# Kernel tuning notes

Hardware: AMD Instinct MI355X
Metric: run time of the kernel (lower is better)

## Reference

```python
import jax, jax.numpy as jnp
import numpy as np

B, T, D = 32, 2048, 128


def setup_inputs() -> dict:
    key = jax.random.key(0)
    k1, k2, k3 = jax.random.split(key, 3)
    values = jax.random.normal(k1, (B, T, D), dtype=jnp.float32)
    # monotonically increasing per-feature timestamps (irregular sampling)
    times = jnp.cumsum(jax.random.uniform(k2, (B, T, D), dtype=jnp.float32), axis=1)
    mask = jax.random.randint(k3, (B, T, D), 0, 2) > 0  # True = observed
    return {"values": values, "times": times, "mask": mask}


def _fill(x, t, mask):
    """Parallel forward fill (LOCF) and backward fill (NOCB) of x and t.

    Replaces the serial Keras RNN scan with cummax/cummin over observation
    indices followed by a gather. Matches ForwardCell semantics:
      forward : x init 0, t init times[:, 0, :]
      backward: x init 0, t init max(times, axis=1)
    """
    Tn = x.shape[1]
    ar = jnp.broadcast_to(jnp.arange(Tn, dtype=jnp.int32)[None, :, None], x.shape)
    # ---- forward fill ----
    fidx = jax.lax.cummax(jnp.where(mask, ar, -1), axis=1)  # last observed idx
    fvalid = fidx >= 0
    fi = jnp.clip(fidx, 0, Tn - 1)
    x_last = jnp.where(fvalid, jnp.take_along_axis(x, fi, axis=1), 0.0)
    t_last = jnp.where(fvalid, jnp.take_along_axis(t, fi, axis=1), t[:, :1, :])
    # ---- backward fill ----
    bidx = jax.lax.cummin(jnp.where(mask, ar, Tn), axis=1, reverse=True)  # next observed idx
    bvalid = bidx < Tn
    bi = jnp.clip(bidx, 0, Tn - 1)
    x_next = jnp.where(bvalid, jnp.take_along_axis(x, bi, axis=1), 0.0)
    t_next = jnp.where(bvalid, jnp.take_along_axis(t, bi, axis=1),
                       jnp.max(t, axis=1, keepdims=True))
    return x_last, t_last, x_next, t_next


def reference(values, times, mask):
    x_last, t_last, x_next, t_next = _fill(values, times, mask)
    denom = t_next - t_last
    num = x_last * (t_next - times) + x_next * (times - t_last)
    safe = denom != 0.0
    x_itp = num / jnp.where(safe, denom, 1.0)
    x_itp = jnp.where(safe & jnp.isfinite(x_itp), x_itp, 0.0)  # nan/inf -> 0
    return jnp.where(mask, values, x_itp)
```

## Files before the change

kernel.cpp:

```cpp
#include <hip/hip_runtime.h>
#include <math.h>

constexpr int B   = 32;
constexpr int T   = 2048;
constexpr int D   = 128;
constexpr int C   = 8;
constexpr int NCH = T / C;
constexpr int DG  = D / 4;

__global__ __launch_bounds__(256)
void linterp_kernel(const float* __restrict__ values,
                    const float* __restrict__ times,
                    const int*   __restrict__ mask,
                    float*       __restrict__ out)
{
    const int gid   = blockIdx.x * 256 + threadIdx.x;
    const int dg    = gid & (DG - 1);
    const int chunk = (gid >> 5) & (NCH - 1);
    const int b     = gid >> 13;

    const int d        = dg * 4;
    const int seq_base = b * T * D + d;
    const int t0i      = chunk * C;

    float4 xv[C], tmv[C], tlv[C];
    unsigned int mb[4] = {0u, 0u, 0u, 0u};
#pragma unroll
    for (int i = 0; i < C; ++i) {
        const int off = seq_base + (t0i + i) * D;
        xv[i]  = *(const float4*)(values + off);
        tmv[i] = *(const float4*)(times + off);
        const int4 m = *(const int4*)(mask + off);
        mb[0] |= (m.x != 0 ? 1u : 0u) << i;
        mb[1] |= (m.y != 0 ? 1u : 0u) << i;
        mb[2] |= (m.z != 0 ? 1u : 0u) << i;
        mb[3] |= (m.w != 0 ? 1u : 0u) << i;
    }

    const float4 t_first4 = *(const float4*)(times + seq_base);
    const float4 t_lastT4 = *(const float4*)(times + seq_base + (T - 1) * D);

    float fx[4] = {0.f, 0.f, 0.f, 0.f};
    float ft[4] = {t_first4.x, t_first4.y, t_first4.z, t_first4.w};
    if (chunk > 0) {
        unsigned int pb[4] = {0u, 0u, 0u, 0u};
#pragma unroll
        for (int i = 0; i < C; ++i) {
            const int4 m = *(const int4*)(mask + seq_base + (t0i - C + i) * D);
            pb[0] |= (m.x != 0 ? 1u : 0u) << i;
            pb[1] |= (m.y != 0 ? 1u : 0u) << i;
            pb[2] |= (m.z != 0 ? 1u : 0u) << i;
            pb[3] |= (m.w != 0 ? 1u : 0u) << i;
        }
#pragma unroll
        for (int j = 0; j < 4; ++j) {
            if (pb[j] != 0u) {
                const int idx = 31 - __builtin_clz(pb[j]);
                const int off = seq_base + (t0i - C + idx) * D + j;
                fx[j] = values[off]; ft[j] = times[off];
            } else {
                for (int t = t0i - C - 1; t >= 0; --t) {
                    const int off = seq_base + t * D + j;
                    if (mask[off] != 0) { fx[j] = values[off]; ft[j] = times[off]; break; }
                }
            }
        }
    }

    float bx[4] = {0.f, 0.f, 0.f, 0.f};
    float bt[4] = {t_lastT4.x, t_lastT4.y, t_lastT4.z, t_lastT4.w};
    if (chunk < NCH - 1) {
        unsigned int nb[4] = {0u, 0u, 0u, 0u};
#pragma unroll
        for (int i = 0; i < C; ++i) {
            const int4 m = *(const int4*)(mask + seq_base + (t0i + C + i) * D);
            nb[0] |= (m.x != 0 ? 1u : 0u) << i;
            nb[1] |= (m.y != 0 ? 1u : 0u) << i;
            nb[2] |= (m.z != 0 ? 1u : 0u) << i;
            nb[3] |= (m.w != 0 ? 1u : 0u) << i;
        }
#pragma unroll
        for (int j = 0; j < 4; ++j) {
            if (nb[j] != 0u) {
                const int idx = __builtin_ctz(nb[j]);
                const int off = seq_base + (t0i + C + idx) * D + j;
                bx[j] = values[off]; bt[j] = times[off];
            } else {
                for (int t = t0i + 2 * C; t < T; ++t) {
                    const int off = seq_base + t * D + j;
                    if (mask[off] != 0) { bx[j] = values[off]; bt[j] = times[off]; break; }
                }
            }
        }
    }

#pragma unroll
    for (int i = 0; i < C; ++i) {
        float* xp = (float*)&xv[i];
        const float* tp = (const float*)&tmv[i];
        float* lp = (float*)&tlv[i];
#pragma unroll
        for (int j = 0; j < 4; ++j) {
            if ((mb[j] >> i) & 1u) { fx[j] = xp[j]; ft[j] = tp[j]; }
            xp[j] = fx[j];
            lp[j] = ft[j];
        }
    }

#pragma unroll
    for (int i = C - 1; i >= 0; --i) {
        const float* xp = (const float*)&xv[i];
        const float* tp = (const float*)&tmv[i];
        const float* lp = (const float*)&tlv[i];
        float4 o;
        float* op = (float*)&o;
#pragma unroll
        for (int j = 0; j < 4; ++j) {
            const bool obs = (mb[j] >> i) & 1u;
            if (obs) { bx[j] = xp[j]; bt[j] = lp[j]; }
            const float denom = bt[j] - lp[j];
            const float num   = xp[j] * (bt[j] - tp[j]) + bx[j] * (tp[j] - lp[j]);
            const bool  safe  = (denom != 0.f);
            float xi = num / (safe ? denom : 1.f);
            xi = (safe && isfinite(xi)) ? xi : 0.f;
            op[j] = obs ? xp[j] : xi;
        }
        *(float4*)(out + seq_base + (t0i + i) * D) = o;
    }
}

extern "C" void kernel_launch(void* const* d_in, const int* in_sizes, int n_in,
                              void* d_out, int out_size, void* d_ws, size_t ws_size,
                              hipStream_t stream)
{
    const float* values = (const float*)d_in[0];
    const float* times  = (const float*)d_in[1];
    const int*   mask   = (const int*)d_in[2];
    float*       out    = (float*)d_out;

    const int total_threads = B * NCH * DG;
    linterp_kernel<<<total_threads / 256, 256, 0, stream>>>(values, times, mask, out);
}
```

Before: 148.3 us.

## Share chunk fill summaries across row groups via LDS with halo rows

Each block now covers a 32-row time tile plus 8-row halos on each side. Eight row-groups each load 6 rows, write per-group last/first observation summaries to shared memory, and combine neighbouring summaries after a barrier. The aim is to replace each thread's redundant global reads of the neighbouring chunk's mask with shared-memory exchange. In exchange, the halo rows are loaded but never written, which adds about 50% more global reads. Only 6 of the 8 row-groups produce output, so a quarter of the threads sit idle during compute.

After: 150.0 us. About the same (+1.1%).

```diff
diff --git a/kernel.cpp b/kernel.cpp
--- a/kernel.cpp
+++ b/kernel.cpp
@@ -4,9 +4,13 @@
 constexpr int B   = 32;
 constexpr int T   = 2048;
 constexpr int D   = 128;
-constexpr int C   = 8;
-constexpr int NCH = T / C;
-constexpr int DG  = D / 4;
+constexpr int TB  = 32;
+constexpr int W   = 8;
+constexpr int RT  = TB + 2 * W;
+constexpr int RG  = 8;
+constexpr int RPT = RT / RG;
+constexpr int DGN = 32;
+constexpr int NT  = T / TB;
 
 __global__ __launch_bounds__(256)
 void linterp_kernel(const float* __restrict__ values,
@@ -14,118 +18,147 @@
                     const int*   __restrict__ mask,
                     float*       __restrict__ out)
 {
-    const int gid   = blockIdx.x * 256 + threadIdx.x;
-    const int dg    = gid & (DG - 1);
-    const int chunk = (gid >> 5) & (NCH - 1);
-    const int b     = gid >> 13;
+    __shared__ float sFX[RG][D];
+    __shared__ float sFT[RG][D];
+    __shared__ float sBX[RG][D];
+    __shared__ float sBT[RG][D];
 
-    const int d        = dg * 4;
-    const int seq_base = b * T * D + d;
-    const int t0i      = chunk * C;
+    const int tid  = threadIdx.x;
+    const int dg   = tid & (DGN - 1);
+    const int rg   = tid >> 5;
+    const int tile = blockIdx.x & (NT - 1);
+    const int b    = blockIdx.x >> 6;
+    const int d    = dg * 4;
+    const int base = b * T * D + d;
+    const int tlo  = tile * TB;
+    const int row0 = tlo - W + rg * RPT;
 
-    float4 xv[C], tmv[C], tlv[C];
+    float4 v[RPT], tv[RPT];
     unsigned int mb[4] = {0u, 0u, 0u, 0u};
 #pragma unroll
-    for (int i = 0; i < C; ++i) {
-        const int off = seq_base + (t0i + i) * D;
-        xv[i]  = *(const float4*)(values + off);
-        tmv[i] = *(const float4*)(times + off);
-        const int4 m = *(const int4*)(mask + off);
-        mb[0] |= (m.x != 0 ? 1u : 0u) << i;
-        mb[1] |= (m.y != 0 ? 1u : 0u) << i;
-        mb[2] |= (m.z != 0 ? 1u : 0u) << i;
-        mb[3] |= (m.w != 0 ? 1u : 0u) << i;
+    for (int i = 0; i < RPT; ++i) {
+        const int r = row0 + i;
+        if (r >= 0 && r < T) {
+            const int off = base + r * D;
+            v[i]  = *(const float4*)(values + off);
+            tv[i] = *(const float4*)(times + off);
+            const int4 m = *(const int4*)(mask + off);
+            mb[0] |= (m.x != 0 ? 1u : 0u) << i;
+            mb[1] |= (m.y != 0 ? 1u : 0u) << i;
+            mb[2] |= (m.z != 0 ? 1u : 0u) << i;
+            mb[3] |= (m.w != 0 ? 1u : 0u) << i;
+        } else {
+            v[i]  = make_float4(0.f, 0.f, 0.f, 0.f);
+            tv[i] = make_float4(0.f, 0.f, 0.f, 0.f);
+        }
     }
 
-    const float4 t_first4 = *(const float4*)(times + seq_base);
-    const float4 t_lastT4 = *(const float4*)(times + seq_base + (T - 1) * D);
+    const float4 tf4 = *(const float4*)(times + base);
+    const float4 te4 = *(const float4*)(times + base + (T - 1) * D);
 
-    float fx[4] = {0.f, 0.f, 0.f, 0.f};
-    float ft[4] = {t_first4.x, t_first4.y, t_first4.z, t_first4.w};
-    if (chunk > 0) {
-        unsigned int pb[4] = {0u, 0u, 0u, 0u};
+    {
+        float fX[4], fT[4], bX[4], bT[4];
 #pragma unroll
-        for (int i = 0; i < C; ++i) {
-            const int4 m = *(const int4*)(mask + seq_base + (t0i - C + i) * D);
-            pb[0] |= (m.x != 0 ? 1u : 0u) << i;
-            pb[1] |= (m.y != 0 ? 1u : 0u) << i;
-            pb[2] |= (m.z != 0 ? 1u : 0u) << i;
-            pb[3] |= (m.w != 0 ? 1u : 0u) << i;
-        }
+        for (int j = 0; j < 4; ++j) { fX[j] = 0.f; fT[j] = -1.f; bX[j] = 0.f; bT[j] = -1.f; }
 #pragma unroll
-        for (int j = 0; j < 4; ++j) {
-            if (pb[j] != 0u) {
-                const int idx = 31 - __builtin_clz(pb[j]);
-                const int off = seq_base + (t0i - C + idx) * D + j;
-                fx[j] = values[off]; ft[j] = times[off];
-            } else {
-                for (int t = t0i - C - 1; t >= 0; --t) {
-                    const int off = seq_base + t * D + j;
-                    if (mask[off] != 0) { fx[j] = values[off]; ft[j] = times[off]; break; }
+        for (int i = 0; i < RPT; ++i) {
+            const float* xp = (const float*)&v[i];
+            const float* tp = (const float*)&tv[i];
+#pragma unroll
+            for (int j = 0; j < 4; ++j) {
+                if ((mb[j] >> i) & 1u) {
+                    fX[j] = xp[j]; fT[j] = tp[j];
+                    if (bT[j] < 0.f) { bX[j] = xp[j]; bT[j] = tp[j]; }
                 }
             }
         }
+        *(float4*)&sFX[rg][d] = make_float4(fX[0], fX[1], fX[2], fX[3]);
+        *(float4*)&sFT[rg][d] = make_float4(fT[0], fT[1], fT[2], fT[3]);
+        *(float4*)&sBX[rg][d] = make_float4(bX[0], bX[1], bX[2], bX[3]);
+        *(float4*)&sBT[rg][d] = make_float4(bT[0], bT[1], bT[2], bT[3]);
     }
+    __syncthreads();
 
-    float bx[4] = {0.f, 0.f, 0.f, 0.f};
-    float bt[4] = {t_lastT4.x, t_lastT4.y, t_lastT4.z, t_lastT4.w};
-    if (chunk < NCH - 1) {
-        unsigned int nb[4] = {0u, 0u, 0u, 0u};
+    const bool has_out = (rg >= 1) && (rg <= 6);
+
+    float cfX[4], cfT[4], cbX[4], cbT[4];
 #pragma unroll
-        for (int i = 0; i < C; ++i) {
-            const int4 m = *(const int4*)(mask + seq_base + (t0i + C + i) * D);
-            nb[0] |= (m.x != 0 ? 1u : 0u) << i;
-            nb[1] |= (m.y != 0 ? 1u : 0u) << i;
-            nb[2] |= (m.z != 0 ? 1u : 0u) << i;
-            nb[3] |= (m.w != 0 ? 1u : 0u) << i;
+    for (int j = 0; j < 4; ++j) { cfX[j] = 0.f; cfT[j] = -1.f; cbX[j] = 0.f; cbT[j] = -1.f; }
+
+    if (has_out) {
+        for (int r2 = 0; r2 < rg; ++r2) {
+            const float4 px = *(const float4*)&sFX[r2][d];
+            const float4 pt = *(const float4*)&sFT[r2][d];
+            const float* pxp = (const float*)&px;
+            const float* ptp = (const float*)&pt;
+#pragma unroll
+            for (int j = 0; j < 4; ++j)
+                if (ptp[j] >= 0.f) { cfX[j] = pxp[j]; cfT[j] = ptp[j]; }
         }
+        for (int r2 = RG - 1; r2 > rg; --r2) {
+            const float4 nx = *(const float4*)&sBX[r2][d];
+            const float4 nt = *(const float4*)&sBT[r2][d];
+            const float* nxp = (const float*)&nx;
+            const float* ntp = (const float*)&nt;
+#pragma unroll
+            for (int j = 0; j < 4; ++j)
+                if (ntp[j] >= 0.f) { cbX[j] = nxp[j]; cbT[j] = ntp[j]; }
+        }
+
 #pragma unroll
         for (int j = 0; j < 4; ++j) {
-            if (nb[j] != 0u) {
-                const int idx = __builtin_ctz(nb[j]);
-                const int off = seq_base + (t0i + C + idx) * D + j;
-                bx[j] = values[off]; bt[j] = times[off];
-            } else {
-                for (int t = t0i + 2 * C; t < T; ++t) {
-                    const int off = seq_base + t * D + j;
-                    if (mask[off] != 0) { bx[j] = values[off]; bt[j] = times[off]; break; }
+            if (cfT[j] < 0.f) {
+                for (int r = tlo - W - 1; r >= 0; --r) {
+                    const int off = base + r * D + j;
+                    if (mask[off] != 0) { cfX[j] = values[off]; cfT[j] = times[off]; break; }
                 }
+                if (cfT[j] < 0.f) { cfX[j] = 0.f; cfT[j] = ((const float*)&tf4)[j]; }
+            }
+            if (cbT[j] < 0.f) {
+                for (int r = tlo + TB + W; r < T; ++r) {
+                    const int off = base + r * D + j;
+                    if (mask[off] != 0) { cbX[j] = values[off]; cbT[j] = times[off]; break; }
+                }
+                if (cbT[j] < 0.f) { cbX[j] = 0.f; cbT[j] = ((const float*)&te4)[j]; }
             }
         }
-    }
+
+        float4 tl[RPT];
+#pragma unroll
+        for (int i = 0; i < RPT; ++i) {
+            float* xp = (float*)&v[i];
+            const float* tp = (const float*)&tv[i];
+            float* lp = (float*)&tl[i];
+#pragma unroll
+            for (int j = 0; j < 4; ++j) {
+                if ((mb[j] >> i) & 1u) { cfX[j] = xp[j]; cfT[j] = tp[j]; }
+                xp[j] = cfX[j];
+                lp[j] = cfT[j];
+            }
+        }
 
 #pragma unroll
-    for (int i = 0; i < C; ++i) {
-        float* xp = (float*)&xv[i];
-        const float* tp = (const float*)&tmv[i];
-        float* lp = (float*)&tlv[i];
+        for (int i = RPT - 1; i >= 0; --i) {
+            const int r = row0 + i;
+            const float* xp = (const float*)&v[i];
+            const float* tp = (const float*)&tv[i];
+            const float* lp = (const float*)&tl[i];
+            float4 o;
+            float* op = (float*)&o;
 #pragma unroll
-        for (int j = 0; j < 4; ++j) {
-            if ((mb[j] >> i) & 1u) { fx[j] = xp[j]; ft[j] = tp[j]; }
-            xp[j] = fx[j];
-            lp[j] = ft[j];
+            for (int j = 0; j < 4; ++j) {
+                const bool obs = (mb[j] >> i) & 1u;
+                if (obs) { cbX[j] = xp[j]; cbT[j] = tp[j]; }
+                const float denom = cbT[j] - lp[j];
+                const float num   = xp[j] * (cbT[j] - tp[j]) + cbX[j] * (tp[j] - lp[j]);
+                const bool  safe  = (denom != 0.f);
+                float xi = num / (safe ? denom : 1.f);
+                xi = (safe && isfinite(xi)) ? xi : 0.f;
+                op[j] = obs ? xp[j] : xi;
+            }
+            if (r >= tlo && r < tlo + TB)
+                *(float4*)(out + base + r * D) = o;
         }
-    }
-
-#pragma unroll
-    for (int i = C - 1; i >= 0; --i) {
-        const float* xp = (const float*)&xv[i];
-        const float* tp = (const float*)&tmv[i];
-        const float* lp = (const float*)&tlv[i];
-        float4 o;
-        float* op = (float*)&o;
-#pragma unroll
-        for (int j = 0; j < 4; ++j) {
-            const bool obs = (mb[j] >> i) & 1u;
-            if (obs) { bx[j] = xp[j]; bt[j] = lp[j]; }
-            const float denom = bt[j] - lp[j];
-            const float num   = xp[j] * (bt[j] - tp[j]) + bx[j] * (tp[j] - lp[j]);
-            const bool  safe  = (denom != 0.f);
-            float xi = num / (safe ? denom : 1.f);
-            xi = (safe && isfinite(xi)) ? xi : 0.f;
-            op[j] = obs ? xp[j] : xi;
-        }
-        *(float4*)(out + seq_base + (t0i + i) * D) = o;
     }
 }
 
@@ -138,6 +171,5 @@
     const int*   mask   = (const int*)d_in[2];
     float*       out    = (float*)d_out;
 
-    const int total_threads = B * NCH * DG;
-    linterp_kernel<<<total_threads / 256, 256, 0, stream>>>(values, times, mask, out);
+    linterp_kernel<<<B * NT, 256, 0, stream>>>(values, times, mask, out);
 }
```
